# Optimization experiments

Hardware: AMD Instinct MI355X
Metric: run time of the kernel (lower is better)

The kernel has to match this reference:

```python
import jax, jax.numpy as jnp
import numpy as np

B, S, E = 1, 4096, 2048
H, HK, D = 16, 4, 128  # num_heads, num_kv_heads, head_dim


def setup_inputs() -> dict:
    key = jax.random.key(0)
    ks = jax.random.split(key, 5)
    sc = 0.02
    return {
        "x": jax.random.normal(ks[0], (B, S, E), dtype=jnp.float32),
        "Wq": jax.random.normal(ks[1], (H * D, E), dtype=jnp.float32) * sc,
        "Wk": jax.random.normal(ks[2], (HK * D, E), dtype=jnp.float32) * sc,
        "Wv": jax.random.normal(ks[3], (HK * D, E), dtype=jnp.float32) * sc,
        "Wo": jax.random.normal(ks[4], (E, H * D), dtype=jnp.float32) * sc,
    }


def reference(x, Wq, Wk, Wv, Wo):
    b, s, _ = x.shape
    # projections (bias=False Linear: x @ W.T), split heads, [B, H, S, D]
    q = (x @ Wq.T).reshape(b, s, H, D).transpose(0, 2, 1, 3).astype(jnp.float16)
    k = (x @ Wk.T).reshape(b, s, HK, D).transpose(0, 2, 1, 3).astype(jnp.float16)
    v = (x @ Wv.T).reshape(b, s, HK, D).transpose(0, 2, 1, 3).astype(jnp.float16)
    # GQA: repeat_interleave kv heads to match query heads
    rep = H // HK
    k = jnp.repeat(k, rep, axis=1)
    v = jnp.repeat(v, rep, axis=1)
    # SDPA in fp32 (non-causal), result cast to half as in torch code
    qf, kf, vf = q.astype(jnp.float32), k.astype(jnp.float32), v.astype(jnp.float32)
    scores = jnp.einsum("bhsd,bhtd->bhst", qf, kf) / np.float32(np.sqrt(D))
    attn = jax.nn.softmax(scores, axis=-1)
    out = jnp.einsum("bhst,bhtd->bhsd", attn, vf).astype(jnp.float16)
    # merge heads and output projection in fp32
    out = out.transpose(0, 2, 1, 3).reshape(b, s, H * D).astype(jnp.float32)
    return out @ Wo.T
```

## Files before the change

kernel.cpp:

```cpp
#include <hip/hip_runtime.h>
#include <stdint.h>

#define SEQ 4096
#define EMB 2048
#define NH 16
#define HDIM 128

typedef _Float16 f16;
typedef _Float16 f16x2 __attribute__((ext_vector_type(2)));
typedef _Float16 f16x4 __attribute__((ext_vector_type(4)));
typedef _Float16 f16x8 __attribute__((ext_vector_type(8)));
typedef float f32x4 __attribute__((ext_vector_type(4)));

#define MFMA16(a, b, c) __builtin_amdgcn_mfma_f32_16x16x32_f16((a), (b), (c), 0, 0, 0)

#define OFF_XH   0ull
#define OFF_WCAT 8388608ull
#define OFF_WHI  14680064ull
#define OFF_WLO  18874368ull
#define OFF_Q    23068672ull
#define OFF_K    31457280ull
#define OFF_VT   33554432ull

__device__ __forceinline__ void gload16(const void* g, void* l) {
    __builtin_amdgcn_global_load_lds((const __attribute__((address_space(1))) unsigned int*)g,
                                     (__attribute__((address_space(3))) unsigned int*)l, 16, 0, 0);
}

__global__ __launch_bounds__(256) void cvt_kernel(
    const float* __restrict__ x, const float* __restrict__ wq,
    const float* __restrict__ wk, const float* __restrict__ wv,
    const float* __restrict__ wo, f16* __restrict__ ws)
{
    int g = blockIdx.x * 256 + threadIdx.x;
    const float* src;
    size_t dst;
    int iswo = 0;
    if (g < 2097152)      { src = x  + (size_t)g * 4;                 dst = OFF_XH + (size_t)g * 4; }
    else if (g < 3145728) { int r = g - 2097152; src = wq + (size_t)r * 4; dst = OFF_WCAT + (size_t)r * 4; }
    else if (g < 3407872) { int r = g - 3145728; src = wk + (size_t)r * 4; dst = OFF_WCAT + 4194304ull + (size_t)r * 4; }
    else if (g < 3670016) { int r = g - 3407872; src = wv + (size_t)r * 4; dst = OFF_WCAT + 5242880ull + (size_t)r * 4; }
    else                  { int r = g - 3670016; src = wo + (size_t)r * 4; dst = OFF_WHI + (size_t)r * 4; iswo = 1; }
    float4 v = *(const float4*)src;
    f16x4 hi;
    hi[0] = (f16)v.x; hi[1] = (f16)v.y; hi[2] = (f16)v.z; hi[3] = (f16)v.w;
    *(f16x4*)&ws[dst] = hi;
    if (iswo) {
        f16x4 lo;
        lo[0] = (f16)(v.x - (float)hi[0]); lo[1] = (f16)(v.y - (float)hi[1]);
        lo[2] = (f16)(v.z - (float)hi[2]); lo[3] = (f16)(v.w - (float)hi[3]);
        *(f16x4*)&ws[dst + (OFF_WLO - OFF_WHI)] = lo;
    }
}

__global__ __launch_bounds__(256) void qkv_gemm(
    const f16* __restrict__ Xh, const f16* __restrict__ Wcat,
    f16* __restrict__ Qb, f16* __restrict__ Kb, f16* __restrict__ Vt)
{
    __shared__ f16 As[128 * 32];
    __shared__ f16 Bs[128 * 32];
    const int tid = threadIdx.x;
    const int lane = tid & 63;
    const int w = tid >> 6;
    const int llo = lane & 15, lhi = lane >> 4;
    const int m0 = blockIdx.y * 128;
    const int n0 = blockIdx.x * 128;
    const int wr = (w >> 1) * 64, wc = (w & 1) * 64;

    f32x4 acc[4][4] = {};

    for (int k0 = 0; k0 < EMB; k0 += 32) {
#pragma unroll
        for (int i = 0; i < 2; ++i) {
            int c = tid + 256 * i;
            gload16(Xh + (size_t)(m0 + (c >> 2)) * EMB + k0 + (c & 3) * 8, &As[c * 8]);
        }
#pragma unroll
        for (int i = 0; i < 2; ++i) {
            int c = tid + 256 * i;
            gload16(Wcat + (size_t)(n0 + (c >> 2)) * EMB + k0 + (c & 3) * 8, &Bs[c * 8]);
        }
        __syncthreads();
        f16x8 af[4], bf[4];
#pragma unroll
        for (int mi = 0; mi < 4; ++mi) af[mi] = *(const f16x8*)&As[(wr + mi * 16 + llo) * 32 + lhi * 8];
#pragma unroll
        for (int ni = 0; ni < 4; ++ni) bf[ni] = *(const f16x8*)&Bs[(wc + ni * 16 + llo) * 32 + lhi * 8];
#pragma unroll
        for (int mi = 0; mi < 4; ++mi)
#pragma unroll
            for (int ni = 0; ni < 4; ++ni)
                acc[mi][ni] = MFMA16(af[mi], bf[ni], acc[mi][ni]);
        __syncthreads();
    }

    if (n0 < 2048) {
#pragma unroll
        for (int mi = 0; mi < 4; ++mi) {
            int m = m0 + wr + mi * 16 + lhi * 4;
#pragma unroll
            for (int ni = 0; ni < 4; ++ni) {
                int n = n0 + wc + ni * 16 + llo;
#pragma unroll
                for (int r = 0; r < 4; ++r)
                    Qb[(size_t)(m + r) * EMB + n] = (f16)acc[mi][ni][r];
            }
        }
    } else if (n0 < 2560) {
#pragma unroll
        for (int mi = 0; mi < 4; ++mi) {
            int m = m0 + wr + mi * 16 + lhi * 4;
#pragma unroll
            for (int ni = 0; ni < 4; ++ni) {
                int n = n0 + wc + ni * 16 + llo - 2048;
#pragma unroll
                for (int r = 0; r < 4; ++r)
                    Kb[(size_t)(m + r) * 512 + n] = (f16)acc[mi][ni][r];
            }
        }
    } else {
#pragma unroll
        for (int mi = 0; mi < 4; ++mi) {
            int mb = m0 + wr + mi * 16 + lhi * 4;
#pragma unroll
            for (int ni = 0; ni < 4; ++ni) {
                int n = n0 + wc + ni * 16 + llo - 2560;
                f16x4 pv;
#pragma unroll
                for (int r = 0; r < 4; ++r) pv[r] = (f16)acc[mi][ni][r];
                *(f16x4*)&Vt[(size_t)n * SEQ + mb] = pv;
            }
        }
    }
}

__global__ __launch_bounds__(256, 2) void attn_kernel(
    const f16* __restrict__ Qb, const f16* __restrict__ Kb, const f16* __restrict__ Vt,
    f16* __restrict__ AO)
{
    __shared__ f16 Ks[2][32 * 128];
    __shared__ f16 Vs[2][128 * 32];
    const int tid = threadIdx.x, lane = tid & 63, w = tid >> 6;
    const int llo = lane & 15, lhi = lane >> 4;
    const int h = blockIdx.y, hk = h >> 2;
    const int wm0 = blockIdx.x * 128 + w * 32;
    const int hcol = h * HDIM;
    const float CS = 0.08838834764831845f * 1.4426950408889634f;

    f16x8 qf[2][4];
#pragma unroll
    for (int G = 0; G < 2; ++G)
#pragma unroll
        for (int kk = 0; kk < 4; ++kk)
            qf[G][kk] = *(const f16x8*)&Qb[(size_t)(wm0 + G * 16 + llo) * EMB + hcol + kk * 32 + lhi * 8];

    float mrun[2] = { -3.0e38f, -3.0e38f };
    float lrun[2] = { 0.f, 0.f };
    f32x4 acc[2][8] = {};

    auto stage = [&](int buf, int t0) {
#pragma unroll
        for (int i = 0; i < 2; ++i) {
            int c = tid + 256 * i;
            int row = c >> 4, sc = c & 15;
            int cc = sc ^ (row & 7);
            gload16(Kb + (size_t)(t0 + row) * 512 + hk * HDIM + cc * 8, &Ks[buf][c * 8]);
        }
#pragma unroll
        for (int i = 0; i < 2; ++i) {
            int c = tid + 256 * i;
            int row = c >> 2, sc = c & 3;
            int cc = sc ^ (row & 3);
            gload16(Vt + (size_t)(hk * HDIM + row) * SEQ + t0 + cc * 8, &Vs[buf][c * 8]);
        }
    };

    stage(0, 0);
    __syncthreads();

    for (int tt = 0; tt < 128; ++tt) {
        int cur = tt & 1;
        if (tt < 127) stage(cur ^ 1, (tt + 1) * 32);

        f32x4 s[2][2] = {};
#pragma unroll
        for (int kk = 0; kk < 4; ++kk) {
            f16x8 kf0, kf1;
            { int row = llo;      int ccs = (kk * 4 + lhi) ^ (row & 7); kf0 = *(const f16x8*)&Ks[cur][row * 128 + ccs * 8]; }
            { int row = 16 + llo; int ccs = (kk * 4 + lhi) ^ (row & 7); kf1 = *(const f16x8*)&Ks[cur][row * 128 + ccs * 8]; }
            s[0][0] = MFMA16(kf0, qf[0][kk], s[0][0]);
            s[0][1] = MFMA16(kf1, qf[0][kk], s[0][1]);
            s[1][0] = MFMA16(kf0, qf[1][kk], s[1][0]);
            s[1][1] = MFMA16(kf1, qf[1][kk], s[1][1]);
        }

        float tm[2];
#pragma unroll
        for (int G = 0; G < 2; ++G) {
            float t = -3.0e38f;
#pragma unroll
            for (int hh = 0; hh < 2; ++hh)
#pragma unroll
                for (int r = 0; r < 4; ++r) { float v = s[G][hh][r] * CS; s[G][hh][r] = v; t = fmaxf(t, v); }
            t = fmaxf(t, __shfl_xor(t, 16, 64));
            t = fmaxf(t, __shfl_xor(t, 32, 64));
            tm[G] = t;
        }
        int need = (tm[0] > mrun[0]) || (tm[1] > mrun[1]);
        if (__any(need)) {
#pragma unroll
            for (int G = 0; G < 2; ++G) {
                float mnew = fmaxf(mrun[G], tm[G]);
                float alpha = __builtin_amdgcn_exp2f(mrun[G] - mnew);
                mrun[G] = mnew; lrun[G] *= alpha;
                float ar[4];
#pragma unroll
                for (int r = 0; r < 4; ++r) ar[r] = __shfl(alpha, lhi * 4 + r, 64);
#pragma unroll
                for (int ni = 0; ni < 8; ++ni)
#pragma unroll
                    for (int r = 0; r < 4; ++r) acc[G][ni][r] *= ar[r];
            }
        }

        union F2U { f16x2 h; uint32_t u; };
        uint32_t pk[2][2][2];
#pragma unroll
        for (int G = 0; G < 2; ++G) {
            float ts = 0.f;
#pragma unroll
            for (int hh = 0; hh < 2; ++hh) {
#pragma unroll
                for (int r = 0; r < 4; ++r) { float p = __builtin_amdgcn_exp2f(s[G][hh][r] - mrun[G]); s[G][hh][r] = p; ts += p; }
                F2U a, b;
                a.h[0] = (f16)s[G][hh][0]; a.h[1] = (f16)s[G][hh][1];
                b.h[0] = (f16)s[G][hh][2]; b.h[1] = (f16)s[G][hh][3];
                pk[G][hh][0] = a.u; pk[G][hh][1] = b.u;
            }
            ts += __shfl_xor(ts, 16, 64);
            ts += __shfl_xor(ts, 32, 64);
            lrun[G] += ts;
        }

        f16x8 paf[2];
#pragma unroll
        for (int G = 0; G < 2; ++G) {
            union { f16x8 v; uint32_t u[4]; } pa;
#pragma unroll
            for (int jj = 0; jj < 4; ++jj) {
                int src = llo + 16 * ((2 * lhi + (jj >> 1)) & 3);
                uint32_t v0 = (uint32_t)__shfl((int)pk[G][0][jj & 1], src, 64);
                uint32_t v1 = (uint32_t)__shfl((int)pk[G][1][jj & 1], src, 64);
                pa.u[jj] = (lhi >= 2) ? v1 : v0;
            }
            paf[G] = pa.v;
        }

#pragma unroll
        for (int ni = 0; ni < 8; ++ni) {
            int d = ni * 16 + llo;
            f16x8 vf = *(const f16x8*)&Vs[cur][d * 32 + ((lhi ^ (d & 3)) * 8)];
            acc[0][ni] = MFMA16(paf[0], vf, acc[0][ni]);
            acc[1][ni] = MFMA16(paf[1], vf, acc[1][ni]);
        }

        __syncthreads();
    }

#pragma unroll
    for (int G = 0; G < 2; ++G) {
        float linv = 1.0f / lrun[G];
        float lr[4];
#pragma unroll
        for (int r = 0; r < 4; ++r) lr[r] = __shfl(linv, lhi * 4 + r, 64);
#pragma unroll
        for (int ni = 0; ni < 8; ++ni) {
            int n = hcol + ni * 16 + llo;
#pragma unroll
            for (int r = 0; r < 4; ++r)
                AO[(size_t)(wm0 + G * 16 + lhi * 4 + r) * EMB + n] = (f16)(acc[G][ni][r] * lr[r]);
        }
    }
}

__global__ __launch_bounds__(256) void o_gemm(
    const f16* __restrict__ A, const f16* __restrict__ Whi, const f16* __restrict__ Wlo,
    float* __restrict__ Co)
{
    __shared__ f16 As[128 * 32];
    __shared__ f16 Bh[128 * 32];
    __shared__ f16 Bl[128 * 32];
    const int tid = threadIdx.x;
    const int lane = tid & 63;
    const int w = tid >> 6;
    const int llo = lane & 15, lhi = lane >> 4;
    const int m0 = blockIdx.y * 128;
    const int n0 = blockIdx.x * 128;
    const int wr = (w >> 1) * 64, wc = (w & 1) * 64;

    f32x4 acc[4][4] = {};

    for (int k0 = 0; k0 < EMB; k0 += 32) {
#pragma unroll
        for (int i = 0; i < 2; ++i) {
            int c = tid + 256 * i;
            gload16(A + (size_t)(m0 + (c >> 2)) * EMB + k0 + (c & 3) * 8, &As[c * 8]);
        }
#pragma unroll
        for (int i = 0; i < 2; ++i) {
            int c = tid + 256 * i;
            gload16(Whi + (size_t)(n0 + (c >> 2)) * EMB + k0 + (c & 3) * 8, &Bh[c * 8]);
        }
#pragma unroll
        for (int i = 0; i < 2; ++i) {
            int c = tid + 256 * i;
            gload16(Wlo + (size_t)(n0 + (c >> 2)) * EMB + k0 + (c & 3) * 8, &Bl[c * 8]);
        }
        __syncthreads();
        f16x8 af[4], bh[4], bl[4];
#pragma unroll
        for (int mi = 0; mi < 4; ++mi) af[mi] = *(const f16x8*)&As[(wr + mi * 16 + llo) * 32 + lhi * 8];
#pragma unroll
        for (int ni = 0; ni < 4; ++ni) bh[ni] = *(const f16x8*)&Bh[(wc + ni * 16 + llo) * 32 + lhi * 8];
#pragma unroll
        for (int ni = 0; ni < 4; ++ni) bl[ni] = *(const f16x8*)&Bl[(wc + ni * 16 + llo) * 32 + lhi * 8];
#pragma unroll
        for (int mi = 0; mi < 4; ++mi)
#pragma unroll
            for (int ni = 0; ni < 4; ++ni) {
                acc[mi][ni] = MFMA16(af[mi], bh[ni], acc[mi][ni]);
                acc[mi][ni] = MFMA16(af[mi], bl[ni], acc[mi][ni]);
            }
        __syncthreads();
    }

#pragma unroll
    for (int mi = 0; mi < 4; ++mi) {
        int m = m0 + wr + mi * 16 + lhi * 4;
#pragma unroll
        for (int ni = 0; ni < 4; ++ni) {
            int n = n0 + wc + ni * 16 + llo;
#pragma unroll
            for (int r = 0; r < 4; ++r)
                Co[(size_t)(m + r) * EMB + n] = acc[mi][ni][r];
        }
    }
}

extern "C" void kernel_launch(void* const* d_in, const int* in_sizes, int n_in,
                              void* d_out, int out_size, void* d_ws, size_t ws_size,
                              hipStream_t stream) {
    const float* x  = (const float*)d_in[0];
    const float* wq = (const float*)d_in[1];
    const float* wk = (const float*)d_in[2];
    const float* wv = (const float*)d_in[3];
    const float* wo = (const float*)d_in[4];
    f16* ws = (f16*)d_ws;

    f16* Xh   = ws + OFF_XH;
    f16* Wcat = ws + OFF_WCAT;
    f16* Whi  = ws + OFF_WHI;
    f16* Wlo  = ws + OFF_WLO;
    f16* Qb   = ws + OFF_Q;
    f16* Kb   = ws + OFF_K;
    f16* Vt   = ws + OFF_VT;

    cvt_kernel<<<18432, 256, 0, stream>>>(x, wq, wk, wv, wo, ws);
    qkv_gemm<<<dim3(24, 32), 256, 0, stream>>>(Xh, Wcat, Qb, Kb, Vt);
    attn_kernel<<<dim3(32, 16), 256, 0, stream>>>(Qb, Kb, Vt, Xh );
    o_gemm<<<dim3(16, 32), 256, 0, stream>>>(Xh , Whi, Wlo, (float*)d_out);
}
```

Measured before the change: 463.0 us.

## Double KV tile size in attention and use permlane swaps for softmax shuffles

The attention kernel now processes 64 keys per iteration instead of 32, with larger double-buffered K/V shared tiles and a wider XOR swizzle. This halves the loop trip count and the per-tile barriers and softmax rescale checks. Row reductions and the P-fragment relayout now use permlane16/32 swap builtins, falling back to shuffles, instead of ds_bpermute-based __shfl. Global source pointers are precomputed outside the loop, and s_setprio raises priority around the MFMA blocks. The larger tiles double the LDS footprint and raise register pressure, which could hurt occupancy at two blocks per CU.

```diff
diff --git a/kernel.cpp b/kernel.cpp
--- a/kernel.cpp
+++ b/kernel.cpp
@@ -11,6 +11,7 @@
 typedef _Float16 f16x4 __attribute__((ext_vector_type(4)));
 typedef _Float16 f16x8 __attribute__((ext_vector_type(8)));
 typedef float f32x4 __attribute__((ext_vector_type(4)));
+typedef unsigned u32x2 __attribute__((ext_vector_type(2)));
 
 #define MFMA16(a, b, c) __builtin_amdgcn_mfma_f32_16x16x32_f16((a), (b), (c), 0, 0, 0)
 
@@ -25,6 +26,47 @@
 __device__ __forceinline__ void gload16(const void* g, void* l) {
     __builtin_amdgcn_global_load_lds((const __attribute__((address_space(1))) unsigned int*)g,
                                      (__attribute__((address_space(3))) unsigned int*)l, 16, 0, 0);
+}
+
+__device__ __forceinline__ void swap32p(uint32_t& x, uint32_t& y) {
+#if __has_builtin(__builtin_amdgcn_permlane32_swap)
+    u32x2 r = __builtin_amdgcn_permlane32_swap(x, y, false, false);
+    x = r[0]; y = r[1];
+#else
+    int l = __lane_id();
+    uint32_t xs = (uint32_t)__shfl_xor((int)x, 32, 64), ys = (uint32_t)__shfl_xor((int)y, 32, 64);
+    uint32_t nx = (l < 32) ? x : ys;
+    uint32_t ny = (l < 32) ? xs : y;
+    x = nx; y = ny;
+#endif
+}
+__device__ __forceinline__ void swap16p(uint32_t& x, uint32_t& y) {
+#if __has_builtin(__builtin_amdgcn_permlane16_swap)
+    u32x2 r = __builtin_amdgcn_permlane16_swap(x, y, false, false);
+    x = r[0]; y = r[1];
+#else
+    int l = __lane_id();
+    uint32_t xs = (uint32_t)__shfl_xor((int)x, 16, 64), ys = (uint32_t)__shfl_xor((int)y, 16, 64);
+    uint32_t nx = (l & 16) ? ys : x;
+    uint32_t ny = (l & 16) ? y : xs;
+    x = nx; y = ny;
+#endif
+}
+__device__ __forceinline__ float red_max_lhi(float t) {
+    uint32_t a = __float_as_uint(t), b = a;
+    swap16p(a, b);
+    t = fmaxf(__uint_as_float(a), __uint_as_float(b));
+    a = __float_as_uint(t); b = a;
+    swap32p(a, b);
+    return fmaxf(__uint_as_float(a), __uint_as_float(b));
+}
+__device__ __forceinline__ float red_sum_lhi(float t) {
+    uint32_t a = __float_as_uint(t), b = a;
+    swap16p(a, b);
+    t = __uint_as_float(a) + __uint_as_float(b);
+    a = __float_as_uint(t); b = a;
+    swap32p(a, b);
+    return __uint_as_float(a) + __uint_as_float(b);
 }
 
 __global__ __launch_bounds__(256) void cvt_kernel(
@@ -138,8 +180,8 @@
     const f16* __restrict__ Qb, const f16* __restrict__ Kb, const f16* __restrict__ Vt,
     f16* __restrict__ AO)
 {
-    __shared__ f16 Ks[2][32 * 128];
-    __shared__ f16 Vs[2][128 * 32];
+    __shared__ f16 Ks[2][64 * 128];
+    __shared__ f16 Vs[2][128 * 64];
     const int tid = threadIdx.x, lane = tid & 63, w = tid >> 6;
     const int llo = lane & 15, lhi = lane >> 4;
     const int h = blockIdx.y, hk = h >> 2;
@@ -154,57 +196,69 @@
         for (int kk = 0; kk < 4; ++kk)
             qf[G][kk] = *(const f16x8*)&Qb[(size_t)(wm0 + G * 16 + llo) * EMB + hcol + kk * 32 + lhi * 8];
 
+    const f16* kgp[4];
+    const f16* vgp[4];
+#pragma unroll
+    for (int i = 0; i < 4; ++i) {
+        int c = tid + 256 * i;
+        int row = c >> 4, cc = (c & 15) ^ (row & 7);
+        kgp[i] = Kb + (size_t)row * 512 + hk * HDIM + cc * 8;
+    }
+#pragma unroll
+    for (int i = 0; i < 4; ++i) {
+        int c = tid + 256 * i;
+        int row = c >> 3, cc = (c & 7) ^ (row & 7);
+        vgp[i] = Vt + (size_t)(hk * HDIM + row) * SEQ + cc * 8;
+    }
+
     float mrun[2] = { -3.0e38f, -3.0e38f };
     float lrun[2] = { 0.f, 0.f };
     f32x4 acc[2][8] = {};
 
     auto stage = [&](int buf, int t0) {
 #pragma unroll
-        for (int i = 0; i < 2; ++i) {
-            int c = tid + 256 * i;
-            int row = c >> 4, sc = c & 15;
-            int cc = sc ^ (row & 7);
-            gload16(Kb + (size_t)(t0 + row) * 512 + hk * HDIM + cc * 8, &Ks[buf][c * 8]);
-        }
-#pragma unroll
-        for (int i = 0; i < 2; ++i) {
-            int c = tid + 256 * i;
-            int row = c >> 2, sc = c & 3;
-            int cc = sc ^ (row & 3);
-            gload16(Vt + (size_t)(hk * HDIM + row) * SEQ + t0 + cc * 8, &Vs[buf][c * 8]);
-        }
+        for (int i = 0; i < 4; ++i)
+            gload16(kgp[i] + (size_t)t0 * 512, &Ks[buf][(tid + 256 * i) * 8]);
+#pragma unroll
+        for (int i = 0; i < 4; ++i)
+            gload16(vgp[i] + t0, &Vs[buf][(tid + 256 * i) * 8]);
     };
 
     stage(0, 0);
     __syncthreads();
 
-    for (int tt = 0; tt < 128; ++tt) {
+    for (int tt = 0; tt < 64; ++tt) {
         int cur = tt & 1;
-        if (tt < 127) stage(cur ^ 1, (tt + 1) * 32);
-
-        f32x4 s[2][2] = {};
+        if (tt < 63) stage(cur ^ 1, (tt + 1) * 64);
+
+        f32x4 s[2][4] = {};
+        __builtin_amdgcn_s_setprio(1);
 #pragma unroll
         for (int kk = 0; kk < 4; ++kk) {
-            f16x8 kf0, kf1;
-            { int row = llo;      int ccs = (kk * 4 + lhi) ^ (row & 7); kf0 = *(const f16x8*)&Ks[cur][row * 128 + ccs * 8]; }
-            { int row = 16 + llo; int ccs = (kk * 4 + lhi) ^ (row & 7); kf1 = *(const f16x8*)&Ks[cur][row * 128 + ccs * 8]; }
-            s[0][0] = MFMA16(kf0, qf[0][kk], s[0][0]);
-            s[0][1] = MFMA16(kf1, qf[0][kk], s[0][1]);
-            s[1][0] = MFMA16(kf0, qf[1][kk], s[1][0]);
-            s[1][1] = MFMA16(kf1, qf[1][kk], s[1][1]);
-        }
+            f16x8 kf[4];
+#pragma unroll
+            for (int hh = 0; hh < 4; ++hh) {
+                int row = llo + 16 * hh;
+                int ccs = (kk * 4 + lhi) ^ (row & 7);
+                kf[hh] = *(const f16x8*)&Ks[cur][row * 128 + ccs * 8];
+            }
+#pragma unroll
+            for (int hh = 0; hh < 4; ++hh) {
+                s[0][hh] = MFMA16(kf[hh], qf[0][kk], s[0][hh]);
+                s[1][hh] = MFMA16(kf[hh], qf[1][kk], s[1][hh]);
+            }
+        }
+        __builtin_amdgcn_s_setprio(0);
 
         float tm[2];
 #pragma unroll
         for (int G = 0; G < 2; ++G) {
             float t = -3.0e38f;
 #pragma unroll
-            for (int hh = 0; hh < 2; ++hh)
+            for (int hh = 0; hh < 4; ++hh)
 #pragma unroll
                 for (int r = 0; r < 4; ++r) { float v = s[G][hh][r] * CS; s[G][hh][r] = v; t = fmaxf(t, v); }
-            t = fmaxf(t, __shfl_xor(t, 16, 64));
-            t = fmaxf(t, __shfl_xor(t, 32, 64));
-            tm[G] = t;
+            tm[G] = red_max_lhi(t);
         }
         int need = (tm[0] > mrun[0]) || (tm[1] > mrun[1]);
         if (__any(need)) {
@@ -224,45 +278,49 @@
         }
 
         union F2U { f16x2 h; uint32_t u; };
-        uint32_t pk[2][2][2];
+        uint32_t Y[2][4][2];
 #pragma unroll
         for (int G = 0; G < 2; ++G) {
             float ts = 0.f;
 #pragma unroll
-            for (int hh = 0; hh < 2; ++hh) {
+            for (int hh = 0; hh < 4; ++hh) {
 #pragma unroll
                 for (int r = 0; r < 4; ++r) { float p = __builtin_amdgcn_exp2f(s[G][hh][r] - mrun[G]); s[G][hh][r] = p; ts += p; }
                 F2U a, b;
                 a.h[0] = (f16)s[G][hh][0]; a.h[1] = (f16)s[G][hh][1];
                 b.h[0] = (f16)s[G][hh][2]; b.h[1] = (f16)s[G][hh][3];
-                pk[G][hh][0] = a.u; pk[G][hh][1] = b.u;
-            }
-            ts += __shfl_xor(ts, 16, 64);
-            ts += __shfl_xor(ts, 32, 64);
-            lrun[G] += ts;
-        }
-
-        f16x8 paf[2];
-#pragma unroll
-        for (int G = 0; G < 2; ++G) {
-            union { f16x8 v; uint32_t u[4]; } pa;
-#pragma unroll
-            for (int jj = 0; jj < 4; ++jj) {
-                int src = llo + 16 * ((2 * lhi + (jj >> 1)) & 3);
-                uint32_t v0 = (uint32_t)__shfl((int)pk[G][0][jj & 1], src, 64);
-                uint32_t v1 = (uint32_t)__shfl((int)pk[G][1][jj & 1], src, 64);
-                pa.u[jj] = (lhi >= 2) ? v1 : v0;
-            }
-            paf[G] = pa.v;
-        }
-
-#pragma unroll
-        for (int ni = 0; ni < 8; ++ni) {
-            int d = ni * 16 + llo;
-            f16x8 vf = *(const f16x8*)&Vs[cur][d * 32 + ((lhi ^ (d & 3)) * 8)];
-            acc[0][ni] = MFMA16(paf[0], vf, acc[0][ni]);
-            acc[1][ni] = MFMA16(paf[1], vf, acc[1][ni]);
-        }
+                Y[G][hh][0] = a.u; Y[G][hh][1] = b.u;
+            }
+            lrun[G] += red_sum_lhi(ts);
+        }
+
+        f16x8 paf[2][2];
+#pragma unroll
+        for (int G = 0; G < 2; ++G)
+#pragma unroll
+            for (int c = 0; c < 2; ++c) {
+                union { f16x8 v; uint32_t u[4]; } pa;
+#pragma unroll
+                for (int jj = 0; jj < 2; ++jj) {
+                    uint32_t xa = Y[G][2 * c][jj], xb = Y[G][2 * c + 1][jj];
+                    swap32p(xa, xb);
+                    swap16p(xa, xb);
+                    pa.u[jj] = xa; pa.u[2 + jj] = xb;
+                }
+                paf[G][c] = pa.v;
+            }
+
+        __builtin_amdgcn_s_setprio(1);
+#pragma unroll
+        for (int c = 0; c < 2; ++c)
+#pragma unroll
+            for (int ni = 0; ni < 8; ++ni) {
+                int d = ni * 16 + llo;
+                f16x8 vf = *(const f16x8*)&Vs[cur][d * 64 + (((4 * c + lhi) ^ (d & 7)) * 8)];
+                acc[0][ni] = MFMA16(paf[0][c], vf, acc[0][ni]);
+                acc[1][ni] = MFMA16(paf[1][c], vf, acc[1][ni]);
+            }
+        __builtin_amdgcn_s_setprio(0);
 
         __syncthreads();
     }
```

New measurement: 430.9 us. -6.9%, faster.
